# Kernel tuning notes

Hardware: AMD Instinct MI355X
Metric: run time of the kernel (lower is better)

## Reference

```python
import jax, jax.numpy as jnp
import numpy as np

B, T, M, D = 2, 2048, 2048, 128
H = M // D
ROTARY_BASE = 10000
NORM_EPS = 1e-6
QK_SCALE = 1.0 / D  # mult = sqrt(qk_scale) applied to both q and k
INFTY_APPROX = 1e30


def setup_inputs() -> dict:
    key = jax.random.key(0)
    ks = jax.random.split(key, 6)
    w_scale = M ** (-0.5)
    return {
        "x": jax.random.normal(ks[0], (B, T, M), jnp.float32),
        "wq": jax.random.normal(ks[1], (M, H, D), jnp.float32) * w_scale,
        "wk": jax.random.normal(ks[2], (M, H, D), jnp.float32) * w_scale,
        "wv": jax.random.normal(ks[3], (M, H, D), jnp.float32) * w_scale,
        "wo": jax.random.normal(ks[4], (H, D, M), jnp.float32) * w_scale,
        "gq": jnp.zeros((H, 1, D), jnp.float32),
        "bq": jnp.zeros((H, 1, D), jnp.float32),
        "gk": jnp.zeros((H, 1, D), jnp.float32),
        "bk": jnp.zeros((H, 1, D), jnp.float32),
    }


def _qk_layernorm(x, g, b):
    # x: [B,H,T,D]; g,b: [H,1,D]; centered RMS norm with trainable (1+g), b
    x = x - jnp.mean(x, axis=-1, keepdims=True)
    x = x / jnp.sqrt(jnp.mean(jnp.square(x), axis=-1, keepdims=True) + NORM_EPS)
    return x * (1.0 + g)[None] + b[None]


def _rotary(x):
    # x: [B,H,T,D]; half-split rotary encoding
    half = D // 2
    positions = jnp.arange(T, dtype=jnp.float32)[:, None]          # [T,1]
    ang_freqs = jnp.power(float(ROTARY_BASE), -jnp.arange(half, dtype=jnp.float32) / half)[None, :]  # [1,half]
    radians = positions * ang_freqs                                  # [T,half]
    cos = jnp.cos(radians)[None, None].astype(x.dtype)               # [1,1,T,half]
    sin = jnp.sin(radians)[None, None].astype(x.dtype)
    even, odd = jnp.split(x, 2, axis=-1)
    return jnp.concatenate([even * cos - odd * sin, even * sin + odd * cos], axis=-1)


def reference(x, wq, wk, wv, wo, gq, bq, gk, bk):
    q = jnp.einsum('bim,mhd->bhid', x, wq)
    k = jnp.einsum('bim,mhd->bhid', x, wk)
    v = jnp.einsum('bim,mhd->bhid', x, wv)
    q = _rotary(_qk_layernorm(q, gq, bq))
    k = _rotary(_qk_layernorm(k, gk, bk))
    mult = jnp.asarray(QK_SCALE ** 0.5, dtype=x.dtype)
    s = jnp.einsum('bhid,bhjd->bhij', q * mult, k * mult)            # [B,H,T,T]
    i = jnp.arange(T)[:, None]
    j = jnp.arange(T)[None, :]
    future = (i < j)[None, None]                                      # mask future positions
    s = s - jnp.asarray(INFTY_APPROX, dtype=s.dtype) * future
    p = jax.nn.softmax(s, axis=-1)
    o = jnp.einsum('bhij,bhjd->bhid', p, v)
    return jnp.einsum('bhid,hdm->bim', o, wo)
```

## Files before the change

### kernel.cpp

```cpp
#include <hip/hip_runtime.h>


#define NB 2
#define NT 2048
#define NM 2048
#define NH 16
#define ND 128

typedef __attribute__((ext_vector_type(4))) float f32x4;
typedef __attribute__((ext_vector_type(8))) short bf16x8;
typedef __attribute__((ext_vector_type(4))) short bf16x4;

#define AS1 __attribute__((address_space(1)))
#define AS3 __attribute__((address_space(3)))

#define SW(r) (((r) ^ ((r) >> 2)) & 3)

__device__ __forceinline__ unsigned short f2bf(float f){
  unsigned int u = __float_as_uint(f);
  u = (u + 0x7fffu + ((u >> 16) & 1u)) >> 16;
  return (unsigned short)u;
}
__device__ __forceinline__ float bf2f(short s){
  return __uint_as_float(((unsigned int)(unsigned short)s) << 16);
}
__device__ __forceinline__ float wredsum(float v){
  #pragma unroll
  for (int m = 1; m < 64; m <<= 1) v += __shfl_xor(v, m);
  return v;
}
__device__ __forceinline__ void gload_lds16(const void* g, void* l){
  __builtin_amdgcn_global_load_lds((const AS1 void*)g, (AS3 void*)l, 16, 0, 0);
}

__global__ __launch_bounds__(256) void prep_k(const float* __restrict__ x,
                                              const float* __restrict__ wq,
                                              const float* __restrict__ wk,
                                              const float* __restrict__ wv,
                                              const float* __restrict__ wo,
                                              short* __restrict__ xb,
                                              short* __restrict__ wT,
                                              float* __restrict__ ctab,
                                              float* __restrict__ stab){
  __shared__ float tl[32][33];
  const int bid = blockIdx.x, tid = threadIdx.x;
  if (bid < 8192){
    size_t gid = (size_t)bid * 256 + tid;
    float4 v = *(const float4*)(x + gid * 4);
    bf16x4 o;
    o[0] = (short)f2bf(v.x); o[1] = (short)f2bf(v.y);
    o[2] = (short)f2bf(v.z); o[3] = (short)f2bf(v.w);
    *(bf16x4*)(xb + gid * 4) = o;
  } else if (bid < 24576){
    int tb = bid - 8192;
    int z = tb >> 12, rem = tb & 4095;
    int n0 = (rem & 63) * 32, k0 = (rem >> 6) * 32;
    const float* src = (z == 0) ? wq : (z == 1) ? wk : (z == 2) ? wv : wo;
    short* dst = wT + (size_t)z * 2048 * 2048;
    int cx = tid & 31, ry = tid >> 5;
    #pragma unroll
    for (int p = 0; p < 4; ++p)
      tl[ry + 8 * p][cx] = src[(size_t)(k0 + ry + 8 * p) * 2048 + n0 + cx];
    __syncthreads();
    #pragma unroll
    for (int p = 0; p < 4; ++p)
      dst[(size_t)(n0 + ry + 8 * p) * 2048 + k0 + cx] =
          (short)f2bf(tl[cx][ry + 8 * p]);
  } else {
    int t = (bid - 24576) * 4 + (tid >> 6);
    int i = tid & 63;
    float freq = __expf(-(float)i * (9.210340371976184f / 64.0f));
    float ang = (float)t * freq;
    ctab[t * 64 + i] = cosf(ang);
    stab[t * 64 + i] = sinf(ang);
  }
}

#define NKT2 64
__global__ __launch_bounds__(512, 4) void gemm256_k(const short* __restrict__ A,
                                                    const short* __restrict__ Bt,
                                                    short* __restrict__ Cq){
  extern __shared__ char lds[];
  const int tid = threadIdx.x;
  const int wid = tid >> 6, lane = tid & 63;
  const int lrow = lane & 15, g8 = lane >> 4;
  const int wm = wid >> 1, wn = wid & 1;
  const int Kdim = 2048;

  int bid = blockIdx.x;
  int s = (bid & 7) * 96 + (bid >> 3);
  const int bx = s & 15;
  const int by = s >> 4;
  const int m0 = bx * 256, n0 = by * 128;

  const int ar = lane >> 2;
  const int ag = (lane & 3) ^ SW(ar);
  const short* Ab = A  + (size_t)(m0 + wid * 32 + ar) * Kdim + ag * 8;
  const short* Bb = Bt + (size_t)(n0 + wid * 16 + ar) * Kdim + ag * 8;

  f32x4 acc[4][4] = {};

  auto STAGE = [&](int c, int kt){
    #pragma unroll
    for (int i = 0; i < 2; ++i)
      gload_lds16(Ab + (size_t)(i * 16) * Kdim + kt * 32,
                  lds + c * 16384 + wid * 2048 + i * 1024);
    gload_lds16(Bb + kt * 32, lds + 32768 + c * 8192 + wid * 1024);
  };
  auto ldA = [&](int c, int mi) -> bf16x8 {
    int row = wm * 64 + mi * 16 + lrow;
    return *(const bf16x8*)(lds + c * 16384 + row * 64 + ((g8 ^ SW(row)) << 4));
  };
  auto ldB = [&](int c, int ni) -> bf16x8 {
    int row = wn * 64 + ni * 16 + lrow;
    return *(const bf16x8*)(lds + 32768 + c * 8192 + row * 64 + ((g8 ^ SW(row)) << 4));
  };

  STAGE(0, 0);

  for (int kt = 0; kt < NKT2; ++kt){
    const int c = kt & 1;
    asm volatile("s_waitcnt vmcnt(0)" ::: "memory");
    __builtin_amdgcn_s_barrier();
    if (kt + 1 < NKT2) STAGE(c ^ 1, kt + 1);

    bf16x8 af[4], bfv[4];
    #pragma unroll
    for (int mi = 0; mi < 4; ++mi) af[mi] = ldA(c, mi);
    #pragma unroll
    for (int ni = 0; ni < 4; ++ni) bfv[ni] = ldB(c, ni);
    #pragma unroll
    for (int mi = 0; mi < 4; ++mi)
      #pragma unroll
      for (int ni = 0; ni < 4; ++ni)
        acc[mi][ni] = __builtin_amdgcn_mfma_f32_16x16x32_bf16(
            af[mi], bfv[ni], acc[mi][ni], 0, 0, 0);
  }

  const int tsel = by >> 4;
  short* dst = Cq + (size_t)tsel * (NB * NH * NT * ND);
  if (tsel < 2){
    #pragma unroll
    for (int mi = 0; mi < 4; ++mi){
      int rowb = m0 + wm * 64 + mi * 16 + g8 * 4;
      #pragma unroll
      for (int ni = 0; ni < 4; ++ni){
        int col = n0 + wn * 64 + ni * 16 + lrow;
        int hd = col & 2047;
        int hh = hd >> 7, d = hd & 127;
        f32x4 a = acc[mi][ni];
        #pragma unroll
        for (int r = 0; r < 4; ++r){
          int bt = rowb + r;
          int b = bt >> 11, t = bt & 2047;
          dst[(((size_t)(b * NH + hh)) * NT + t) * ND + d] = (short)f2bf(a[r]);
        }
      }
    }
  } else {
    #pragma unroll
    for (int mi = 0; mi < 4; ++mi){
      int rowb = m0 + wm * 64 + mi * 16 + g8 * 4;
      int b = rowb >> 11, t0 = rowb & 2047;
      int jb = t0 >> 6, toff = t0 & 63;
      #pragma unroll
      for (int ni = 0; ni < 4; ++ni){
        int col = n0 + wn * 64 + ni * 16 + lrow;
        int hd = col & 2047;
        int hh = hd >> 7, d = hd & 127;
        f32x4 a = acc[mi][ni];
        bf16x4 w4;
        #pragma unroll
        for (int r = 0; r < 4; ++r) w4[r] = (short)f2bf(a[r]);
        *(bf16x4*)&dst[(((size_t)(b * NH + hh) * 32 + jb) * ND + d) * 64 + toff] = w4;
      }
    }
  }
}

__global__ __launch_bounds__(512, 4) void gemmo_k(const short* __restrict__ A,
                                                  const short* __restrict__ Bt,
                                                  float* __restrict__ Cout){
  extern __shared__ char lds[];
  const int tid = threadIdx.x;
  const int wid = tid >> 6, lane = tid & 63;
  const int lrow = lane & 15, g8 = lane >> 4;
  const int wm = wid >> 1, wn = wid & 1;
  const int Kdim = 2048;

  int bid = blockIdx.x;
  int s = (bid & 7) * 32 + (bid >> 3);
  const int bx = s & 15;
  const int by = s >> 4;
  const int m0 = bx * 256, n0 = by * 128;

  const int ar = lane >> 2;
  const int ag = (lane & 3) ^ SW(ar);
  const short* Ab = A  + (size_t)(m0 + wid * 32 + ar) * Kdim + ag * 8;
  const short* Bb = Bt + (size_t)(n0 + wid * 16 + ar) * Kdim + ag * 8;

  f32x4 acc[4][4] = {};

  auto STAGE = [&](int c, int kt){
    #pragma unroll
    for (int i = 0; i < 2; ++i)
      gload_lds16(Ab + (size_t)(i * 16) * Kdim + kt * 32,
                  lds + c * 16384 + wid * 2048 + i * 1024);
    gload_lds16(Bb + kt * 32, lds + 32768 + c * 8192 + wid * 1024);
  };
  auto ldA = [&](int c, int mi) -> bf16x8 {
    int row = wm * 64 + mi * 16 + lrow;
    return *(const bf16x8*)(lds + c * 16384 + row * 64 + ((g8 ^ SW(row)) << 4));
  };
  auto ldB = [&](int c, int ni) -> bf16x8 {
    int row = wn * 64 + ni * 16 + lrow;
    return *(const bf16x8*)(lds + 32768 + c * 8192 + row * 64 + ((g8 ^ SW(row)) << 4));
  };

  STAGE(0, 0);

  for (int kt = 0; kt < NKT2; ++kt){
    const int c = kt & 1;
    asm volatile("s_waitcnt vmcnt(0)" ::: "memory");
    __builtin_amdgcn_s_barrier();
    if (kt + 1 < NKT2) STAGE(c ^ 1, kt + 1);

    bf16x8 af[4], bfv[4];
    #pragma unroll
    for (int mi = 0; mi < 4; ++mi) af[mi] = ldA(c, mi);
    #pragma unroll
    for (int ni = 0; ni < 4; ++ni) bfv[ni] = ldB(c, ni);
    #pragma unroll
    for (int mi = 0; mi < 4; ++mi)
      #pragma unroll
      for (int ni = 0; ni < 4; ++ni)
        acc[mi][ni] = __builtin_amdgcn_mfma_f32_16x16x32_bf16(
            af[mi], bfv[ni], acc[mi][ni], 0, 0, 0);
  }

  #pragma unroll
  for (int mi = 0; mi < 4; ++mi){
    int rowb = m0 + wm * 64 + mi * 16 + g8 * 4;
    #pragma unroll
    for (int ni = 0; ni < 4; ++ni){
      int col = n0 + wn * 64 + ni * 16 + lrow;
      f32x4 a = acc[mi][ni];
      #pragma unroll
      for (int r = 0; r < 4; ++r)
        Cout[(size_t)(rowb + r) * 2048 + col] = a[r];
    }
  }
}

__global__ __launch_bounds__(256) void norm_rope_k(const short* __restrict__ qkv,
                                                   short* __restrict__ outp,
                                                   const float* __restrict__ gq,
                                                   const float* __restrict__ bq,
                                                   const float* __restrict__ gk,
                                                   const float* __restrict__ bk,
                                                   const float* __restrict__ ctab,
                                                   const float* __restrict__ stab){
  int which = blockIdx.y;
  const short* src = qkv + (size_t)which * (NB * NH * NT * ND);
  short* dst = outp + (size_t)which * (NB * NH * NT * ND);
  const float* g = which ? gk : gq;
  const float* bb = which ? bk : bq;
  const float qs = which ? 1.0f : 0.011271055007f;
  int wid = threadIdx.x >> 6, lane = threadIdx.x & 63;
  size_t row = (size_t)blockIdx.x * 4 + wid;
  int h = (int)((row >> 11) & 15);
  int t = (int)(row & 2047);
  const short* rp = src + row * ND;
  float v0 = bf2f(rp[lane]), v1 = bf2f(rp[lane + 64]);
  float mean = wredsum(v0 + v1) * (1.0f / 128.0f);
  float c0 = v0 - mean, c1 = v1 - mean;
  float ms = wredsum(c0 * c0 + c1 * c1) * (1.0f / 128.0f);
  float rstd = rsqrtf(ms + 1e-6f);
  float n0 = c0 * rstd * (1.0f + g[h * ND + lane]) + bb[h * ND + lane];
  float n1 = c1 * rstd * (1.0f + g[h * ND + lane + 64]) + bb[h * ND + lane + 64];
  float co = ctab[t * 64 + lane], si = stab[t * 64 + lane];
  short* wp = dst + row * ND;
  wp[lane]      = (short)f2bf((n0 * co - n1 * si) * qs);
  wp[lane + 64] = (short)f2bf((n0 * si + n1 * co) * qs);
}

__global__ __launch_bounds__(512) void attn_k(const short* __restrict__ qn,
                                              const short* __restrict__ kn,
                                              const short* __restrict__ vt,
                                              short* __restrict__ ob){
  extern __shared__ char lds[];
  const int tid = threadIdx.x;
  const int wid = tid >> 6, lane = tid & 63;
  const int lrow = lane & 15, g8 = lane >> 4;
  const int id = blockIdx.x;
  const int qs = id >> 5;
  const int bh = id & 31;
  const int b = bh >> 4, h = bh & 15;
  const size_t base = (size_t)bh * NT * ND;
  char* Pw = lds + 98304 + wid * 2048;

  auto STAGE = [&](int jb){
    const int cb = jb % 3;
    #pragma unroll
    for (int i = 0; i < 2; ++i){
      int r0 = wid * 4 + i * 32;
      int r = r0 + (lane >> 4);
      int g = lane & 15;
      gload_lds16(kn + base + (size_t)(jb * 64 + r) * ND + ((g ^ (r & 7)) << 3),
                  lds + cb * 16384 + r0 * 256);
    }
    #pragma unroll
    for (int i = 0; i < 2; ++i){
      int d0 = wid * 8 + i * 64;
      int d = d0 + (lane >> 3);
      int g = lane & 7;
      gload_lds16(vt + base + (size_t)jb * 8192 + d * 64 + ((g ^ (d & 7)) << 3),
                  lds + 49152 + cb * 16384 + d0 * 128);
    }
  };

  for (int pass = 0; pass < 2; ++pass){
    const int qt = pass ? (15 - qs) : qs;
    const int t0 = qt * 128;
    const int wrow0 = t0 + wid * 16;
    const int tq = wrow0 + lrow;
    bf16x8 qf[4];
    #pragma unroll
    for (int dc = 0; dc < 4; ++dc)
      qf[dc] = *(const bf16x8*)(qn + base + (size_t)tq * ND + dc * 32 + g8 * 8);
    f32x4 O[8] = {};
    float m = -3e38f, lsum = 0.0f;
    const int ntiles = 2 * qt + 2;

    __syncthreads();
    STAGE(0);
    STAGE(1);

    for (int jb = 0; jb < ntiles; ++jb){
      if (jb + 1 < ntiles) asm volatile("s_waitcnt vmcnt(4)" ::: "memory");
      else                 asm volatile("s_waitcnt vmcnt(0)" ::: "memory");
      __builtin_amdgcn_s_barrier();
      if (jb + 2 < ntiles) STAGE(jb + 2);
      const char* Kb = lds + (jb % 3) * 16384;
      const char* Vb = lds + 49152 + (jb % 3) * 16384;

      if (jb * 64 <= wrow0 + 15){
        f32x4 st[4] = {};
        __builtin_amdgcn_s_setprio(1);
        #pragma unroll
        for (int dc = 0; dc < 4; ++dc)
          #pragma unroll
          for (int js = 0; js < 4; ++js){
            int jl = js * 16 + lrow;
            bf16x8 kf = *(const bf16x8*)(Kb + jl * 256 +
                          (((dc * 4 + g8) ^ (jl & 7)) << 4));
            st[js] = __builtin_amdgcn_mfma_f32_16x16x32_bf16(kf, qf[dc], st[js], 0, 0, 0);
          }
        __builtin_amdgcn_s_setprio(0);
        if (jb * 64 + 63 > wrow0){
          #pragma unroll
          for (int js = 0; js < 4; ++js)
            #pragma unroll
            for (int r = 0; r < 4; ++r){
              int j = jb * 64 + js * 16 + g8 * 4 + r;
              if (j > tq) st[js][r] = -3e38f;
            }
        }
        f32x4 m4 = st[0];
        #pragma unroll
        for (int js = 1; js < 4; ++js)
          #pragma unroll
          for (int r = 0; r < 4; ++r) m4[r] = fmaxf(m4[r], st[js][r]);
        float mx = fmaxf(fmaxf(m4[0], m4[1]), fmaxf(m4[2], m4[3]));
        mx = fmaxf(mx, __shfl_xor(mx, 16));
        mx = fmaxf(mx, __shfl_xor(mx, 32));
        if (!__all(mx <= m + 8.0f)){
          float mnew = fmaxf(m, mx);
          float fac = exp2f(m - mnew);
          m = mnew;
          lsum *= fac;
          #pragma unroll
          for (int dcb = 0; dcb < 8; ++dcb) O[dcb] *= fac;
        }
        float ps = 0.0f;
        #pragma unroll
        for (int js = 0; js < 4; ++js){
          float p0 = exp2f(st[js][0] - m);
          float p1 = exp2f(st[js][1] - m);
          float p2 = exp2f(st[js][2] - m);
          float p3 = exp2f(st[js][3] - m);
          ps += (p0 + p1) + (p2 + p3);
          unsigned int lo, hi;
          asm("v_cvt_pk_bf16_f32 %0, %1, %2" : "=v"(lo) : "v"(p0), "v"(p1));
          asm("v_cvt_pk_bf16_f32 %0, %1, %2" : "=v"(hi) : "v"(p2), "v"(p3));
          uint2 w; w.x = lo; w.y = hi;
          *(uint2*)(Pw + lrow * 128 + ((js * 32 + g8 * 8) ^ ((lrow & 7) << 4))) = w;
        }
        ps += __shfl_xor(ps, 16);
        ps += __shfl_xor(ps, 32);
        lsum += ps;
        asm volatile("s_waitcnt lgkmcnt(0)" ::: "memory");
        __builtin_amdgcn_s_setprio(1);
        #pragma unroll
        for (int j32 = 0; j32 < 2; ++j32){
          bf16x8 pf = *(const bf16x8*)(Pw + lrow * 128 +
                        ((j32 * 64 + g8 * 16) ^ ((lrow & 7) << 4)));
          #pragma unroll
          for (int dcb = 0; dcb < 8; ++dcb){
            int d = dcb * 16 + lrow;
            bf16x8 vf = *(const bf16x8*)(Vb + d * 128 +
                          (((j32 * 4 + g8) ^ (d & 7)) << 4));
            O[dcb] = __builtin_amdgcn_mfma_f32_16x16x32_bf16(vf, pf, O[dcb], 0, 0, 0);
          }
        }
        __builtin_amdgcn_s_setprio(0);
      }
    }
    float inv = 1.0f / lsum;
    #pragma unroll
    for (int dcb = 0; dcb < 8; ++dcb){
      bf16x4 w4;
      #pragma unroll
      for (int r = 0; r < 4; ++r) w4[r] = (short)f2bf(O[dcb][r] * inv);
      *(bf16x4*)(ob + ((size_t)(b * NT + tq)) * (NH * ND) + h * ND + dcb * 16 + g8 * 4) = w4;
    }
  }
}

extern "C" void kernel_launch(void* const* d_in, const int* in_sizes, int n_in,
                              void* d_out, int out_size, void* d_ws, size_t ws_size,
                              hipStream_t stream){
  const float* x  = (const float*)d_in[0];
  const float* wq = (const float*)d_in[1];
  const float* wk = (const float*)d_in[2];
  const float* wv = (const float*)d_in[3];
  const float* wo = (const float*)d_in[4];
  const float* gq = (const float*)d_in[5];
  const float* bq = (const float*)d_in[6];
  const float* gk = (const float*)d_in[7];
  const float* bk = (const float*)d_in[8];

  char* ws = (char*)d_ws;
  short* xb   = (short*)(ws);
  short* wT   = (short*)(ws + 16777216);
  short* qkvb = (short*)(ws + 50331648);
  short* qkn  = (short*)(ws + 100663296);
  short* ob   = (short*)(ws + 134217728);
  float* ctab = (float*)(ws + 150994944);
  float* stab = (float*)(ws + 151519232);

  (void)hipFuncSetAttribute((const void*)gemm256_k,
                            hipFuncAttributeMaxDynamicSharedMemorySize, 49152);
  (void)hipFuncSetAttribute((const void*)gemmo_k,
                            hipFuncAttributeMaxDynamicSharedMemorySize, 49152);
  (void)hipFuncSetAttribute((const void*)attn_k,
                            hipFuncAttributeMaxDynamicSharedMemorySize, 114688);

  prep_k<<<dim3(25088), dim3(256), 0, stream>>>(x, wq, wk, wv, wo, xb, wT, ctab, stab);
  gemm256_k<<<dim3(768), dim3(512), 49152, stream>>>(xb, wT, qkvb);
  norm_rope_k<<<dim3(16384, 2), dim3(256), 0, stream>>>(qkvb, qkn, gq, bq, gk, bk, ctab, stab);
  attn_k<<<dim3(256), dim3(512), 114688, stream>>>(qkn, qkn + 8388608,
                                                   qkvb + 2 * (size_t)8388608, ob);
  gemmo_k<<<dim3(256), dim3(512), 49152, stream>>>(ob, wT + 3 * (size_t)4194304,
                                                   (float*)d_out);
}
```

Before: 272.2 us.

## Fuse QK layernorm and rotary into the QKV projection GEMM epilogue

Removes the separate norm_rope kernel. The QKV GEMM epilogue now computes per-row mean and variance across the 128-wide head tile using shuffles plus an LDS reduction, applies the norm, swaps rotary partner halves through LDS, and writes normalized q/k directly. This drops one bf16 round trip of q/k through global memory and one kernel launch. In exchange the GEMM needs more LDS (raised to 72KB), which can cut occupancy. Variance now uses E[x^2]-mean^2 in fp32 rather than a centered two-pass form.

```diff
diff --git a/kernel.cpp b/kernel.cpp
--- a/kernel.cpp
+++ b/kernel.cpp
@@ -23,11 +23,6 @@
 }
 __device__ __forceinline__ float bf2f(short s){
   return __uint_as_float(((unsigned int)(unsigned short)s) << 16);
-}
-__device__ __forceinline__ float wredsum(float v){
-  #pragma unroll
-  for (int m = 1; m < 64; m <<= 1) v += __shfl_xor(v, m);
-  return v;
 }
 __device__ __forceinline__ void gload_lds16(const void* g, void* l){
   __builtin_amdgcn_global_load_lds((const AS1 void*)g, (AS3 void*)l, 16, 0, 0);
@@ -79,7 +74,14 @@
 #define NKT2 64
 __global__ __launch_bounds__(512, 4) void gemm256_k(const short* __restrict__ A,
                                                     const short* __restrict__ Bt,
-                                                    short* __restrict__ Cq){
+                                                    short* __restrict__ Cq,
+                                                    short* __restrict__ Cn,
+                                                    const float* __restrict__ gq,
+                                                    const float* __restrict__ bq,
+                                                    const float* __restrict__ gk,
+                                                    const float* __restrict__ bk,
+                                                    const float* __restrict__ ctab,
+                                                    const float* __restrict__ stab){
   extern __shared__ char lds[];
   const int tid = threadIdx.x;
   const int wid = tid >> 6, lane = tid & 63;
@@ -138,26 +140,75 @@
   }
 
   const int tsel = by >> 4;
-  short* dst = Cq + (size_t)tsel * (NB * NH * NT * ND);
+  const int hh = by & 15;
   if (tsel < 2){
-    #pragma unroll
-    for (int mi = 0; mi < 4; ++mi){
-      int rowb = m0 + wm * 64 + mi * 16 + g8 * 4;
-      #pragma unroll
-      for (int ni = 0; ni < 4; ++ni){
-        int col = n0 + wn * 64 + ni * 16 + lrow;
-        int hd = col & 2047;
-        int hh = hd >> 7, d = hd & 127;
-        f32x4 a = acc[mi][ni];
-        #pragma unroll
-        for (int r = 0; r < 4; ++r){
-          int bt = rowb + r;
-          int b = bt >> 11, t = bt & 2047;
-          dst[(((size_t)(b * NH + hh)) * NT + t) * ND + d] = (short)f2bf(a[r]);
+    const float* gv = tsel ? gk : gq;
+    const float* bv = tsel ? bk : bq;
+    float* red = (float*)lds;
+    short* xch = (short*)(lds + 4096);
+    __syncthreads();
+    #pragma unroll
+    for (int mi = 0; mi < 4; ++mi)
+      #pragma unroll
+      for (int r = 0; r < 4; ++r){
+        float a0 = acc[mi][0][r], a1 = acc[mi][1][r];
+        float a2 = acc[mi][2][r], a3 = acc[mi][3][r];
+        float s1 = (a0 + a1) + (a2 + a3);
+        float s2 = (a0*a0 + a1*a1) + (a2*a2 + a3*a3);
+        #pragma unroll
+        for (int off = 1; off < 16; off <<= 1){
+          s1 += __shfl_xor(s1, off);
+          s2 += __shfl_xor(s2, off);
+        }
+        if (lrow == 0){
+          int row = wm * 64 + mi * 16 + g8 * 4 + r;
+          red[row * 4 + wn * 2]     = s1;
+          red[row * 4 + wn * 2 + 1] = s2;
         }
       }
-    }
+    __syncthreads();
+    #pragma unroll
+    for (int mi = 0; mi < 4; ++mi)
+      #pragma unroll
+      for (int r = 0; r < 4; ++r){
+        int row = wm * 64 + mi * 16 + g8 * 4 + r;
+        float s1 = red[row * 4] + red[row * 4 + 2];
+        float s2 = red[row * 4 + 1] + red[row * 4 + 3];
+        float mean = s1 * (1.0f / 128.0f);
+        float var = s2 * (1.0f / 128.0f) - mean * mean;
+        float rstd = rsqrtf(var + 1e-6f);
+        #pragma unroll
+        for (int ni = 0; ni < 4; ++ni){
+          int d = wn * 64 + ni * 16 + lrow;
+          float n = (acc[mi][ni][r] - mean) * rstd * (1.0f + gv[hh * 128 + d])
+                    + bv[hh * 128 + d];
+          acc[mi][ni][r] = n;
+          xch[row * 136 + d] = (short)f2bf(n);
+        }
+      }
+    __syncthreads();
+    const float sgn = wn ? 1.0f : -1.0f;
+    const float qsc = tsel ? 1.0f : 0.011271055007f;
+    short* dstn = Cn + (size_t)tsel * (NB * NH * NT * ND);
+    #pragma unroll
+    for (int mi = 0; mi < 4; ++mi)
+      #pragma unroll
+      for (int r = 0; r < 4; ++r){
+        int rowb = m0 + wm * 64 + mi * 16 + g8 * 4 + r;
+        int b = rowb >> 11, t = rowb & 2047;
+        int row = rowb - m0;
+        #pragma unroll
+        for (int ni = 0; ni < 4; ++ni){
+          int d = wn * 64 + ni * 16 + lrow;
+          int dl = ni * 16 + lrow;
+          float pv = bf2f(xch[row * 136 + (d ^ 64)]);
+          float c = ctab[t * 64 + dl], sn = stab[t * 64 + dl];
+          float o = (acc[mi][ni][r] * c + sgn * pv * sn) * qsc;
+          dstn[(((size_t)(b * NH + hh)) * NT + t) * ND + d] = (short)f2bf(o);
+        }
+      }
   } else {
+    short* dst = Cq + 2 * (size_t)(NB * NH * NT * ND);
     #pragma unroll
     for (int mi = 0; mi < 4; ++mi){
       int rowb = m0 + wm * 64 + mi * 16 + g8 * 4;
@@ -165,9 +216,7 @@
       int jb = t0 >> 6, toff = t0 & 63;
       #pragma unroll
       for (int ni = 0; ni < 4; ++ni){
-        int col = n0 + wn * 64 + ni * 16 + lrow;
-        int hd = col & 2047;
-        int hh = hd >> 7, d = hd & 127;
+        int d = wn * 64 + ni * 16 + lrow;
         f32x4 a = acc[mi][ni];
         bf16x4 w4;
         #pragma unroll
@@ -250,38 +299,6 @@
         Cout[(size_t)(rowb + r) * 2048 + col] = a[r];
     }
   }
-}
-
-__global__ __launch_bounds__(256) void norm_rope_k(const short* __restrict__ qkv,
-                                                   short* __restrict__ outp,
-                                                   const float* __restrict__ gq,
-                                                   const float* __restrict__ bq,
-                                                   const float* __restrict__ gk,
-                                                   const float* __restrict__ bk,
-                                                   const float* __restrict__ ctab,
-                                                   const float* __restrict__ stab){
-  int which = blockIdx.y;
-  const short* src = qkv + (size_t)which * (NB * NH * NT * ND);
-  short* dst = outp + (size_t)which * (NB * NH * NT * ND);
-  const float* g = which ? gk : gq;
-  const float* bb = which ? bk : bq;
-  const float qs = which ? 1.0f : 0.011271055007f;
-  int wid = threadIdx.x >> 6, lane = threadIdx.x & 63;
-  size_t row = (size_t)blockIdx.x * 4 + wid;
-  int h = (int)((row >> 11) & 15);
-  int t = (int)(row & 2047);
-  const short* rp = src + row * ND;
-  float v0 = bf2f(rp[lane]), v1 = bf2f(rp[lane + 64]);
-  float mean = wredsum(v0 + v1) * (1.0f / 128.0f);
-  float c0 = v0 - mean, c1 = v1 - mean;
-  float ms = wredsum(c0 * c0 + c1 * c1) * (1.0f / 128.0f);
-  float rstd = rsqrtf(ms + 1e-6f);
-  float n0 = c0 * rstd * (1.0f + g[h * ND + lane]) + bb[h * ND + lane];
-  float n1 = c1 * rstd * (1.0f + g[h * ND + lane + 64]) + bb[h * ND + lane + 64];
-  float co = ctab[t * 64 + lane], si = stab[t * 64 + lane];
-  short* wp = dst + row * ND;
-  wp[lane]      = (short)f2bf((n0 * co - n1 * si) * qs);
-  wp[lane + 64] = (short)f2bf((n0 * si + n1 * co) * qs);
 }
 
 __global__ __launch_bounds__(512) void attn_k(const short* __restrict__ qn,
@@ -450,15 +467,15 @@
   float* stab = (float*)(ws + 151519232);
 
   (void)hipFuncSetAttribute((const void*)gemm256_k,
-                            hipFuncAttributeMaxDynamicSharedMemorySize, 49152);
+                            hipFuncAttributeMaxDynamicSharedMemorySize, 73728);
   (void)hipFuncSetAttribute((const void*)gemmo_k,
                             hipFuncAttributeMaxDynamicSharedMemorySize, 49152);
   (void)hipFuncSetAttribute((const void*)attn_k,
                             hipFuncAttributeMaxDynamicSharedMemorySize, 114688);
 
   prep_k<<<dim3(25088), dim3(256), 0, stream>>>(x, wq, wk, wv, wo, xb, wT, ctab, stab);
-  gemm256_k<<<dim3(768), dim3(512), 49152, stream>>>(xb, wT, qkvb);
-  norm_rope_k<<<dim3(16384, 2), dim3(256), 0, stream>>>(qkvb, qkn, gq, bq, gk, bk, ctab, stab);
+  gemm256_k<<<dim3(768), dim3(512), 73728, stream>>>(xb, wT, qkvb, qkn,
+                                                     gq, bq, gk, bk, ctab, stab);
   attn_k<<<dim3(256), dim3(512), 114688, stream>>>(qkn, qkn + 8388608,
                                                    qkvb + 2 * (size_t)8388608, ob);
   gemmo_k<<<dim3(256), dim3(512), 49152, stream>>>(ob, wT + 3 * (size_t)4194304,
```

Measured after the change: 262.5 us. 3.6% less time.
